# Kernel optimization log

Hardware: AMD Instinct MI355X
Metric: run time of the kernel (lower is better)

Reference implementation:

```python
import jax, jax.numpy as jnp
import numpy as np

NUM_HEADS = 32
NUM_KV_HEADS = 8
HEAD_DIM = 128


def setup_inputs() -> dict:
    key = jax.random.key(0)
    ks = jax.random.split(key, 5)
    B, S, H = 1, 2048, 4096
    hidden_states = jax.random.normal(ks[0], (B, S, H), dtype=jnp.float32)
    # additive causal mask: 0 on/below diagonal, large negative above
    neg = jnp.finfo(jnp.float32).min
    causal = jnp.where(jnp.tril(jnp.ones((S, S), dtype=bool)), 0.0, neg)
    attention_mask = causal[None, None, :, :].astype(jnp.float32)
    sc = 0.02
    wq = jax.random.normal(ks[1], (NUM_HEADS * HEAD_DIM, H), dtype=jnp.float32) * sc
    wk = jax.random.normal(ks[2], (NUM_KV_HEADS * HEAD_DIM, H), dtype=jnp.float32) * sc
    wv = jax.random.normal(ks[3], (NUM_KV_HEADS * HEAD_DIM, H), dtype=jnp.float32) * sc
    wo = jax.random.normal(ks[4], (H, NUM_HEADS * HEAD_DIM), dtype=jnp.float32) * sc
    return {"hidden_states": hidden_states, "attention_mask": attention_mask,
            "wq": wq, "wk": wk, "wv": wv, "wo": wo}


def reference(hidden_states, attention_mask, wq, wk, wv, wo):
    B, S, H = hidden_states.shape
    groups = NUM_HEADS // NUM_KV_HEADS
    # projections (Linear, no bias): y = x @ W^T
    q = (hidden_states @ wq.T).reshape(B, S, NUM_HEADS, HEAD_DIM).transpose(0, 2, 1, 3)
    k = (hidden_states @ wk.T).reshape(B, S, NUM_KV_HEADS, HEAD_DIM).transpose(0, 2, 1, 3)
    v = (hidden_states @ wv.T).reshape(B, S, NUM_KV_HEADS, HEAD_DIM).transpose(0, 2, 1, 3)
    # GQA: repeat KV heads (matches torch repeat_interleave on head dim)
    k = jnp.repeat(k, groups, axis=1)  # [B, NUM_HEADS, S, D]
    v = jnp.repeat(v, groups, axis=1)
    scale = 1.0 / (HEAD_DIM ** 0.5)
    scores = jnp.einsum('bhqd,bhkd->bhqk', q, k) * scale
    scores = scores + attention_mask
    attn = jax.nn.softmax(scores.astype(jnp.float32), axis=-1).astype(q.dtype)
    out = jnp.einsum('bhqk,bhkd->bhqd', attn, v)  # [B, H, S, D]
    out = out.transpose(0, 2, 1, 3).reshape(B, S, NUM_HEADS * HEAD_DIM)
    return out @ wo.T
```

## Files before the change

kernel.cpp:

```cpp
#include <hip/hip_runtime.h>
#include <hip/hip_bf16.h>
#include <cstdint>
#include <cstddef>

typedef __bf16 bf16;
typedef __bf16 bf16x4 __attribute__((ext_vector_type(4)));
typedef __bf16 bf16x8 __attribute__((ext_vector_type(8)));
typedef float  f32x4  __attribute__((ext_vector_type(4)));

#define S_LEN 2048
#define HID   4096
#define NH    32
#define NKV   8
#define HD    128
#define QLD   6144
#define KVLD  6144

__device__ __forceinline__ void gload_lds16(const bf16* g, bf16* l) {
    __builtin_amdgcn_global_load_lds(
        (const __attribute__((address_space(1))) void*)g,
        (__attribute__((address_space(3))) void*)l,
        16, 0, 0);
}

__global__ void cast_f32_bf16(const float* __restrict__ in, bf16* __restrict__ out, int n4) {
    int idx    = blockIdx.x * blockDim.x + threadIdx.x;
    int stride = gridDim.x * blockDim.x;
    for (int i = idx; i < n4; i += stride) {
        float4 v = ((const float4*)in)[i];
        bf16x4 o = { (bf16)v.x, (bf16)v.y, (bf16)v.z, (bf16)v.w };
        ((bf16x4*)out)[i] = o;
    }
}

template <typename OUT_T>
__global__ __launch_bounds__(256) void gemm_bt(const bf16* __restrict__ A,
                                               const bf16* __restrict__ B,
                                               OUT_T* __restrict__ C,
                                               int M, int N, int K) {
    __shared__ alignas(16) bf16 sA[2][128 * 64];
    __shared__ alignas(16) bf16 sB[2][128 * 64];

    const int tid  = threadIdx.x;
    const int lane = tid & 63;
    const int w    = tid >> 6;
    const int wr   = w >> 1;
    const int wc   = w & 1;
    const int l15  = lane & 15;
    const int l4   = lane >> 4;
    const int m0   = blockIdx.y * 128;
    const int n0   = blockIdx.x * 128;

    f32x4 acc[4][4] = {};

    const int rsub = lane >> 3;
    const int scol = ((lane & 7) * 8) ^ (rsub << 3);

    auto stage = [&](int t, int buf) {
#pragma unroll
        for (int j = 0; j < 4; ++j) {
            const int c   = w * 4 + j;
            const int row = c * 8 + rsub;
            gload_lds16(A + (size_t)(m0 + row) * K + t * 64 + scol, &sA[buf][c * 512]);
            gload_lds16(B + (size_t)(n0 + row) * K + t * 64 + scol, &sB[buf][c * 512]);
        }
    };

    const int nt = K >> 6;

    stage(0, 0);
    __syncthreads();

    int buf = 0;
    for (int t = 0; t < nt; ++t) {
        if (t + 1 < nt) stage(t + 1, buf ^ 1);

        bf16x8 af[2][4], bfr[2][4];
#pragma unroll
        for (int kk = 0; kk < 2; ++kk) {
#pragma unroll
            for (int i = 0; i < 4; ++i) {
                const int ra = wr * 64 + i * 16 + l15;
                af[kk][i]  = *(const bf16x8*)&sA[buf][ra * 64 + ((kk * 32 + l4 * 8) ^ ((ra & 7) << 3))];
                const int rb = wc * 64 + i * 16 + l15;
                bfr[kk][i] = *(const bf16x8*)&sB[buf][rb * 64 + ((kk * 32 + l4 * 8) ^ ((rb & 7) << 3))];
            }
        }
#pragma unroll
        for (int kk = 0; kk < 2; ++kk)
#pragma unroll
            for (int i = 0; i < 4; ++i)
#pragma unroll
                for (int j = 0; j < 4; ++j)
                    acc[i][j] = __builtin_amdgcn_mfma_f32_16x16x32_bf16(af[kk][i], bfr[kk][j], acc[i][j], 0, 0, 0);

        __syncthreads();
        buf ^= 1;
    }

#pragma unroll
    for (int i = 0; i < 4; ++i) {
        const int row = m0 + wr * 64 + i * 16 + l4 * 4;
#pragma unroll
        for (int j = 0; j < 4; ++j) {
            const int col = n0 + wc * 64 + j * 16 + l15;
#pragma unroll
            for (int r = 0; r < 4; ++r)
                C[(size_t)(row + r) * N + col] = (OUT_T)acc[i][j][r];
        }
    }
}

__global__ __launch_bounds__(512) void attn_kernel(const bf16* __restrict__ Q,
                                                   const bf16* __restrict__ Kp,
                                                   const bf16* __restrict__ Vp,
                                                   bf16* __restrict__ O) {
    __shared__ alignas(16) bf16 sK[2][64 * 128];
    __shared__ alignas(16) bf16 sVt[2][128 * 64];
    __shared__ alignas(16) bf16 sP[8][16 * 64];

    const int tid  = threadIdx.x;
    const int lane = tid & 63;
    const int w    = tid >> 6;
    const int l15  = lane & 15;
    const int l4   = lane >> 4;
    const int h    = blockIdx.y;
    const int hk   = h >> 2;
    const int b    = blockIdx.x;
    const int qH   = 15 - b;
    const int qL   = b;
    const float C2 = 0.12751744f;

    const bf16* Kbase = Kp + hk * HD;
    const bf16* Vbase = Vp + hk * HD;

    const int rbH = qH * 128 + w * 16;
    const int rbL = qL * 128 + w * 16;
    bf16x8 qfH[4], qfL[4];
#pragma unroll
    for (int ks = 0; ks < 4; ++ks) {
        qfH[ks] = *(const bf16x8*)(Q + (size_t)(rbH + l15) * QLD + h * HD + ks * 32 + l4 * 8);
        qfL[ks] = *(const bf16x8*)(Q + (size_t)(rbL + l15) * QLD + h * HD + ks * 32 + l4 * 8);
    }

    f32x4 accH[8] = {}, accL[8] = {};
    float lH[4] = {0.f, 0.f, 0.f, 0.f}, lL[4] = {0.f, 0.f, 0.f, 0.f};

    auto stageK = [&](int t, int buf) {
#pragma unroll
        for (int j = 0; j < 2; ++j) {
            const int c   = w * 2 + j;
            const int row = c * 4 + l4;
            const int col = (l15 * 8) ^ ((row & 7) << 3);
            gload_lds16(Kbase + (size_t)(t * 64 + row) * KVLD + col, &sK[buf][c * 512]);
        }
    };
    auto loadV = [&](int t, bf16x8* vr) {
#pragma unroll
        for (int r2 = 0; r2 < 2; ++r2) {
            const int c = r2 * 8 + w;
            vr[r2] = *(const bf16x8*)(Vbase + (size_t)(t * 64 + lane) * KVLD + c * 8);
        }
    };
    auto writeV = [&](const bf16x8* vr, int buf) {
#pragma unroll
        for (int r2 = 0; r2 < 2; ++r2) {
            const int c = r2 * 8 + w;
#pragma unroll
            for (int e = 0; e < 8; ++e) {
                const int row = c * 8 + e;
                sVt[buf][row * 64 + (lane ^ (e << 3))] = vr[r2][e];
            }
        }
    };

    auto strip = [&](const bf16x8* qf, f32x4* acc_o, float* lrow,
                     int rbase, int s0, int cur) {
        if (s0 > rbase + 15) return;
        f32x4 accs[4] = {};
        __builtin_amdgcn_s_setprio(1);
#pragma unroll
        for (int ks = 0; ks < 4; ++ks) {
#pragma unroll
            for (int j = 0; j < 4; ++j) {
                const int krow = j * 16 + l15;
                bf16x8 kb = *(const bf16x8*)&sK[cur][krow * 128 + ((ks * 32 + l4 * 8) ^ ((krow & 7) << 3))];
                accs[j] = __builtin_amdgcn_mfma_f32_16x16x32_bf16(qf[ks], kb, accs[j], 0, 0, 0);
            }
        }
        __builtin_amdgcn_s_setprio(0);

        float sc[4][4];
        float rsum[4] = {0.f, 0.f, 0.f, 0.f};
        const bool needMask = (s0 + 63 > rbase);
        if (needMask) {
#pragma unroll
            for (int j = 0; j < 4; ++j) {
                const int scol = s0 + j * 16 + l15;
#pragma unroll
                for (int i = 0; i < 4; ++i) {
                    const int r = rbase + l4 * 4 + i;
                    const float p = (scol > r) ? 0.f : exp2f(accs[j][i] * C2);
                    sc[j][i] = p;
                    rsum[i] += p;
                }
            }
        } else {
#pragma unroll
            for (int j = 0; j < 4; ++j)
#pragma unroll
                for (int i = 0; i < 4; ++i) {
                    const float p = exp2f(accs[j][i] * C2);
                    sc[j][i] = p;
                    rsum[i] += p;
                }
        }
#pragma unroll
        for (int i = 0; i < 4; ++i) {
#pragma unroll
            for (int msk = 1; msk < 16; msk <<= 1)
                rsum[i] += __shfl_xor(rsum[i], msk);
            lrow[i] += rsum[i];
        }

#pragma unroll
        for (int j = 0; j < 4; ++j)
#pragma unroll
            for (int i = 0; i < 4; ++i) {
                const int prow = l4 * 4 + i;
                const int s2   = (prow & 7) ^ ((prow >> 3) << 1);
                sP[w][prow * 64 + ((j * 16 + l15) ^ (s2 << 3))] = (bf16)sc[j][i];
            }

        __builtin_amdgcn_s_setprio(1);
#pragma unroll
        for (int kk = 0; kk < 2; ++kk) {
            const int s2l = (l15 & 7) ^ ((l15 >> 3) << 1);
            bf16x8 pa = *(const bf16x8*)&sP[w][l15 * 64 + ((kk * 32 + l4 * 8) ^ (s2l << 3))];
#pragma unroll
            for (int d = 0; d < 8; ++d) {
                const int vrow = d * 16 + l15;
                bf16x8 vb = *(const bf16x8*)&sVt[cur][vrow * 64 + ((kk * 32 + l4 * 8) ^ ((vrow & 7) << 3))];
                acc_o[d] = __builtin_amdgcn_mfma_f32_16x16x32_bf16(pa, vb, acc_o[d], 0, 0, 0);
            }
        }
        __builtin_amdgcn_s_setprio(0);
    };

    const int ntH = 2 * qH + 2;
    const int ntL = 2 * qL + 2;

    bf16x8 vreg[2];
    loadV(0, vreg);
    stageK(0, 0);
    writeV(vreg, 0);
    __syncthreads();

    int cur = 0;
    for (int t = 0; t < ntH; ++t) {
        const int s0 = t * 64;
        const bool pf = (t + 1 < ntH);
        if (pf) {
            loadV(t + 1, vreg);
            stageK(t + 1, cur ^ 1);
        }

        strip(qfH, accH, lH, rbH, s0, cur);
        if (t < ntL) strip(qfL, accL, lL, rbL, s0, cur);

        if (pf) writeV(vreg, cur ^ 1);

        __syncthreads();
        cur ^= 1;
    }

    float rH[4], rL[4];
#pragma unroll
    for (int i = 0; i < 4; ++i) { rH[i] = __frcp_rn(lH[i]); rL[i] = __frcp_rn(lL[i]); }
#pragma unroll
    for (int d = 0; d < 8; ++d)
#pragma unroll
        for (int i = 0; i < 4; ++i) {
            O[(size_t)(rbH + l4 * 4 + i) * HID + h * HD + d * 16 + l15] = (bf16)(accH[d][i] * rH[i]);
            O[(size_t)(rbL + l4 * 4 + i) * HID + h * HD + d * 16 + l15] = (bf16)(accL[d][i] * rL[i]);
        }
}

extern "C" void kernel_launch(void* const* d_in, const int* in_sizes, int n_in,
                              void* d_out, int out_size, void* d_ws, size_t ws_size,
                              hipStream_t stream) {
    const float* hx = (const float*)d_in[0];
    const float* wq = (const float*)d_in[2];
    const float* wk = (const float*)d_in[3];
    const float* wv = (const float*)d_in[4];
    const float* wo = (const float*)d_in[5];
    float* out = (float*)d_out;

    bf16* Xb   = (bf16*)d_ws;
    bf16* Wqkv = Xb + 8388608;
    bf16* QKV  = Wqkv + 25165824;

    auto cast = [&](const float* src, bf16* dst, int n) {
        int n4 = n / 4;
        int blocks = (n4 + 255) / 256;
        if (blocks > 2048) blocks = 2048;
        cast_f32_bf16<<<blocks, 256, 0, stream>>>(src, dst, n4);
    };

    cast(hx, Xb, 2048 * 4096);
    cast(wq, Wqkv, 4096 * 4096);
    cast(wk, Wqkv + 16777216, 1024 * 4096);
    cast(wv, Wqkv + 20971520, 1024 * 4096);

    gemm_bt<bf16><<<dim3(48, 16), 256, 0, stream>>>(Xb, Wqkv, QKV, 2048, 6144, 4096);

    cast(wo, Wqkv, 4096 * 4096);

    attn_kernel<<<dim3(8, 32), 512, 0, stream>>>(QKV, QKV + 4096, QKV + 5120, Xb);

    gemm_bt<float><<<dim3(32, 16), 256, 0, stream>>>(Xb, Wqkv, out, 2048, 4096, 4096);
}
```

Baseline: 316.0 us.

## Remap GEMM block order to M-fastest and share K fragments across attention strips

The GEMM launch becomes a 1D grid with the M tile index varying fastest, so consecutive blocks share the same B (weight) column tile and get better L2 reuse of weights. In attention, the QK^T MFMA loops for the high and low query strips are merged so each K fragment read from LDS feeds both strips, halving LDS reads for K. The merge raises register pressure, since two score accumulators are live at once.

Result: slower. 336.3 us (+6.4%).

```diff
diff --git a/kernel.cpp b/kernel.cpp
--- a/kernel.cpp
+++ b/kernel.cpp
@@ -48,8 +48,9 @@
     const int wc   = w & 1;
     const int l15  = lane & 15;
     const int l4   = lane >> 4;
-    const int m0   = blockIdx.y * 128;
-    const int n0   = blockIdx.x * 128;
+    const int mt   = M >> 7;
+    const int m0   = (blockIdx.x % mt) * 128;
+    const int n0   = (blockIdx.x / mt) * 128;
 
     f32x4 acc[4][4] = {};
 
@@ -174,22 +175,8 @@
         }
     };
 
-    auto strip = [&](const bf16x8* qf, f32x4* acc_o, float* lrow,
-                     int rbase, int s0, int cur) {
-        if (s0 > rbase + 15) return;
-        f32x4 accs[4] = {};
-        __builtin_amdgcn_s_setprio(1);
-#pragma unroll
-        for (int ks = 0; ks < 4; ++ks) {
-#pragma unroll
-            for (int j = 0; j < 4; ++j) {
-                const int krow = j * 16 + l15;
-                bf16x8 kb = *(const bf16x8*)&sK[cur][krow * 128 + ((ks * 32 + l4 * 8) ^ ((krow & 7) << 3))];
-                accs[j] = __builtin_amdgcn_mfma_f32_16x16x32_bf16(qf[ks], kb, accs[j], 0, 0, 0);
-            }
-        }
-        __builtin_amdgcn_s_setprio(0);
-
+    auto finish = [&](const f32x4* aS, f32x4* acc_o, float* lrow,
+                      int rbase, int s0, int cur) {
         float sc[4][4];
         float rsum[4] = {0.f, 0.f, 0.f, 0.f};
         const bool needMask = (s0 + 63 > rbase);
@@ -200,7 +187,7 @@
 #pragma unroll
                 for (int i = 0; i < 4; ++i) {
                     const int r = rbase + l4 * 4 + i;
-                    const float p = (scol > r) ? 0.f : exp2f(accs[j][i] * C2);
+                    const float p = (scol > r) ? 0.f : exp2f(aS[j][i] * C2);
                     sc[j][i] = p;
                     rsum[i] += p;
                 }
@@ -210,7 +197,7 @@
             for (int j = 0; j < 4; ++j)
 #pragma unroll
                 for (int i = 0; i < 4; ++i) {
-                    const float p = exp2f(accs[j][i] * C2);
+                    const float p = exp2f(aS[j][i] * C2);
                     sc[j][i] = p;
                     rsum[i] += p;
                 }
@@ -265,8 +252,27 @@
             stageK(t + 1, cur ^ 1);
         }
 
-        strip(qfH, accH, lH, rbH, s0, cur);
-        if (t < ntL) strip(qfL, accL, lL, rbL, s0, cur);
+        const bool actH = (s0 <= rbH + 15);
+        const bool actL = (t < ntL) && (s0 <= rbL + 15);
+
+        f32x4 aH[4] = {}, aL[4] = {};
+        if (actH || actL) {
+            __builtin_amdgcn_s_setprio(1);
+#pragma unroll
+            for (int j = 0; j < 4; ++j) {
+#pragma unroll
+                for (int ks = 0; ks < 4; ++ks) {
+                    const int krow = j * 16 + l15;
+                    bf16x8 kbf = *(const bf16x8*)&sK[cur][krow * 128 + ((ks * 32 + l4 * 8) ^ ((krow & 7) << 3))];
+                    if (actH) aH[j] = __builtin_amdgcn_mfma_f32_16x16x32_bf16(qfH[ks], kbf, aH[j], 0, 0, 0);
+                    if (actL) aL[j] = __builtin_amdgcn_mfma_f32_16x16x32_bf16(qfL[ks], kbf, aL[j], 0, 0, 0);
+                }
+            }
+            __builtin_amdgcn_s_setprio(0);
+        }
+
+        if (actH) finish(aH, accH, lH, rbH, s0, cur);
+        if (actL) finish(aL, accL, lL, rbL, s0, cur);
 
         if (pf) writeV(vreg, cur ^ 1);
 
@@ -312,11 +318,11 @@
     cast(wk, Wqkv + 16777216, 1024 * 4096);
     cast(wv, Wqkv + 20971520, 1024 * 4096);
 
-    gemm_bt<bf16><<<dim3(48, 16), 256, 0, stream>>>(Xb, Wqkv, QKV, 2048, 6144, 4096);
+    gemm_bt<bf16><<<dim3(768), 256, 0, stream>>>(Xb, Wqkv, QKV, 2048, 6144, 4096);
 
     cast(wo, Wqkv, 4096 * 4096);
 
     attn_kernel<<<dim3(8, 32), 512, 0, stream>>>(QKV, QKV + 4096, QKV + 5120, Xb);
 
-    gemm_bt<float><<<dim3(32, 16), 256, 0, stream>>>(Xb, Wqkv, out, 2048, 4096, 4096);
-}
+    gemm_bt<float><<<dim3(512), 256, 0, stream>>>(Xb, Wqkv, out, 2048, 4096, 4096);
+}
```
